# Kernel optimization log

Measured on AMD Instinct MI355X. Metric: run time of the kernel, lower is better.

Reference implementation:

```python
import jax, jax.numpy as jnp
import numpy as np

HEADS = 16
HEAD_DIM = 64
EMBED = HEADS * HEAD_DIM  # 1024
N, L = 4, 4096


def setup_inputs() -> dict:
    key = jax.random.key(0)
    k1, k2, k3, k4, k5, k6, k7, k8 = jax.random.split(key, 8)
    s = 0.02
    return {
        "q": jax.random.normal(k1, (N, L, EMBED), jnp.float32),
        "k": jax.random.normal(k2, (N, L, EMBED), jnp.float32),
        "v": jax.random.normal(k3, (N, L, EMBED), jnp.float32),
        "mask": jnp.ones((N, L, HEADS, HEADS), jnp.int32),
        # torch Linear weights: (out_features, in_features)
        "q_w": jax.random.normal(k4, (HEAD_DIM, HEAD_DIM), jnp.float32) * s,
        "k_w": jax.random.normal(k5, (HEAD_DIM, HEAD_DIM), jnp.float32) * s,
        "v_w": jax.random.normal(k6, (HEAD_DIM, HEAD_DIM), jnp.float32) * s,
        "fc_w": jax.random.normal(k7, (EMBED, EMBED), jnp.float32) * s,
        "fc_b": jax.random.normal(k8, (EMBED,), jnp.float32) * s,
    }


def reference(q, k, v, mask, q_w, k_w, v_w, fc_w, fc_b):
    n, ql = q.shape[0], q.shape[1]
    # reshape to (N, L, H, D) and apply per-head-dim linear projections (x @ W.T)
    q4 = q.reshape(n, ql, HEADS, HEAD_DIM) @ q_w.T
    k4 = k.reshape(n, k.shape[1], HEADS, HEAD_DIM) @ k_w.T
    v4 = v.reshape(n, v.shape[1], HEADS, HEAD_DIM) @ v_w.T
    # Faithful to the original: matmul broadcasts over (N, L), contracting head_dim,
    # so logits are (N, L, H, H) -- attention across heads per token.
    scale = 1.0 / jnp.sqrt(jnp.float32(HEAD_DIM))
    logits = jnp.einsum("nlhd,nlgd->nlhg", q4, k4) * scale
    logits = jnp.where(mask == 0, -jnp.inf, logits)
    weights = jax.nn.softmax(logits, axis=-1)
    out4 = jnp.einsum("nlhg,nlgd->nlhd", weights, v4)  # (N, L, H, D)
    # Faithful scrambled reshape: permute to (N, H, L, D) then flatten to (N, L, H*D)
    out = out4.transpose(0, 2, 1, 3).reshape(n, ql, HEADS * HEAD_DIM)
    return out @ fc_w.T + fc_b
```

## Files before the change

kernel.cpp:

```cpp
#include <hip/hip_runtime.h>
#include <hip/hip_bf16.h>
#include <stdint.h>

#define TOKENS 16384
#define LSEQ 4096
#define WPAD 72

typedef short bf16x8 __attribute__((ext_vector_type(8)));
typedef float f32x4 __attribute__((ext_vector_type(4)));

typedef __attribute__((address_space(1))) void as1_t;
typedef __attribute__((address_space(3))) void as3_t;

__device__ __forceinline__ unsigned short f2bf(float x) {
  __hip_bfloat16 t = __float2bfloat16(x);
  return *reinterpret_cast<unsigned short*>(&t);
}

__device__ __forceinline__ bf16x8 pack8(float4 a, float4 b) {
  bf16x8 t;
  t[0] = (short)f2bf(a.x); t[1] = (short)f2bf(a.y);
  t[2] = (short)f2bf(a.z); t[3] = (short)f2bf(a.w);
  t[4] = (short)f2bf(b.x); t[5] = (short)f2bf(b.y);
  t[6] = (short)f2bf(b.z); t[7] = (short)f2bf(b.w);
  return t;
}

__device__ __forceinline__ void async16(const void* g, void* lds) {
  __builtin_amdgcn_global_load_lds((as1_t*)const_cast<void*>(g),
                                   (as3_t*)lds, 16, 0, 0);
}

__global__ __launch_bounds__(256) void cvt_bf16(const float* __restrict__ s,
                                                unsigned short* __restrict__ d,
                                                int n4) {
  int i = blockIdx.x * 256 + threadIdx.x;
  if (i < n4) {
    float4 f = ((const float4*)s)[i];
    union { unsigned short us[4]; uint2 u2; } pk;
    pk.us[0] = f2bf(f.x); pk.us[1] = f2bf(f.y);
    pk.us[2] = f2bf(f.z); pk.us[3] = f2bf(f.w);
    ((uint2*)d)[i] = pk.u2;
  }
}

__global__ __launch_bounds__(1024) void prep_weights(
    const float* __restrict__ qw, const float* __restrict__ kw,
    const float* __restrict__ vw, unsigned short* __restrict__ Mout,
    unsigned short* __restrict__ vwout) {
  __shared__ float ql[4096], kl[4096];
  const int t = threadIdx.x;
  ((float4*)ql)[t] = ((const float4*)qw)[t];
  ((float4*)kl)[t] = ((const float4*)kw)[t];
  {
    float4 f = ((const float4*)vw)[t];
    union { unsigned short us[4]; uint2 u2; } pk;
    pk.us[0] = f2bf(f.x); pk.us[1] = f2bf(f.y);
    pk.us[2] = f2bf(f.z); pk.us[3] = f2bf(f.w);
    ((uint2*)vwout)[t] = pk.u2;
  }
  __syncthreads();
  const int f = t >> 4;
  const int e0 = (t & 15) * 4;
  float acc0 = 0.f, acc1 = 0.f, acc2 = 0.f, acc3 = 0.f;
#pragma unroll 8
  for (int d = 0; d < 64; ++d) {
    const float qv = ql[d * 64 + f];
    const float4 kv = *(const float4*)&kl[d * 64 + e0];
    acc0 += qv * kv.x; acc1 += qv * kv.y; acc2 += qv * kv.z; acc3 += qv * kv.w;
  }
  union { unsigned short us[4]; uint2 u2; } pk;
  pk.us[0] = f2bf(acc0); pk.us[1] = f2bf(acc1);
  pk.us[2] = f2bf(acc2); pk.us[3] = f2bf(acc3);
  *(uint2*)&Mout[f * 64 + e0] = pk.u2;
}

#define STG_BYTES 13312

__global__ __launch_bounds__(128) void attn7(
    const float* __restrict__ q, const float* __restrict__ k,
    const float* __restrict__ v, const int* __restrict__ mask,
    const unsigned short* __restrict__ Mg, const unsigned short* __restrict__ vwg,
    unsigned short* __restrict__ X) {
  __shared__ unsigned short Ml[64 * WPAD];
  __shared__ unsigned short Vw[64 * WPAD];
  __shared__ char stg_[2][2][STG_BYTES];
  __shared__ char scr_[2][2048];

  const int tid = threadIdx.x;
  const int l = tid & 63, w = tid >> 6;
  const int lr = l & 15, lg = l >> 4;
  char* scr = scr_[w];

  {
    const int row = tid >> 1, c0 = (tid & 1) * 32;
#pragma unroll
    for (int j = 0; j < 4; ++j) {
      *(uint4*)&Ml[row * WPAD + c0 + j * 8] = *(const uint4*)(Mg + row * 64 + c0 + j * 8);
      *(uint4*)&Vw[row * WPAD + c0 + j * 8] = *(const uint4*)(vwg + row * 64 + c0 + j * 8);
    }
  }
  __syncthreads();

  auto issue = [&](int tok, char* dst) {
    const size_t tb = (size_t)tok * 1024;
#pragma unroll
    for (int i = 0; i < 4; ++i) {
      const int r = i * 4 + (l >> 4);
      const int se = r * 64 + (((l & 15) ^ (r & 7)) << 2);
      async16(q + tb + se, dst + i * 1024);
      async16(k + tb + se, dst + 4096 + i * 1024);
      async16(v + tb + se, dst + 8192 + i * 1024);
    }
    async16(mask + (size_t)tok * 256 + l * 4, dst + 12288);
  };

  const int tok0 = (blockIdx.x * 2 + w) * 8;
  issue(tok0, stg_[w][0]);

  const int r7 = lr & 7;
  const int fr0 = lr * 128 + ((lg * 16) ^ (r7 << 4));
  const int fr1 = lr * 128 + ((64 + lg * 16) ^ (r7 << 4));

#pragma unroll
  for (int t = 0; t < 8; ++t) {
    const int tok = tok0 + t;
    char* cur = stg_[w][t & 1];

    if (t < 7) {
      issue(tok + 1, stg_[w][(t + 1) & 1]);
      asm volatile("s_waitcnt vmcnt(13)" ::: "memory");
    } else {
      asm volatile("s_waitcnt vmcnt(2)" ::: "memory");
    }
    __builtin_amdgcn_sched_barrier(0);

    const int4 mk4 = *(const int4*)(cur + 12288 + lr * 64 + lg * 16);
    auto ldfrag = [&](const char* base, int kc) -> bf16x8 {
      const int c0 = kc * 8 + 2 * lg;
      const float4 f0 = *(const float4*)(base + lr * 256 + (((c0) ^ r7) << 4));
      const float4 f1 = *(const float4*)(base + lr * 256 + (((c0 + 1) ^ r7) << 4));
      return pack8(f0, f1);
    };
    const bf16x8 aq0 = ldfrag(cur, 0),        aq1 = ldfrag(cur, 1);
    const bf16x8 ak0 = ldfrag(cur + 4096, 0), ak1 = ldfrag(cur + 4096, 1);
    const bf16x8 av0 = ldfrag(cur + 8192, 0), av1 = ldfrag(cur + 8192, 1);

    f32x4 accu[4], accv[4];
#pragma unroll
    for (int n = 0; n < 4; ++n) {
      const int wrow = (n * 16 + lr) * WPAD;
      f32x4 z = {};
      const bf16x8 bm0 = *(const bf16x8*)&Ml[wrow + lg * 8];
      const bf16x8 bm1 = *(const bf16x8*)&Ml[wrow + 32 + lg * 8];
      accu[n] = __builtin_amdgcn_mfma_f32_16x16x32_bf16(ak0, bm0, z, 0, 0, 0);
      accu[n] = __builtin_amdgcn_mfma_f32_16x16x32_bf16(ak1, bm1, accu[n], 0, 0, 0);
      const bf16x8 bw0 = *(const bf16x8*)&Vw[wrow + lg * 8];
      const bf16x8 bw1 = *(const bf16x8*)&Vw[wrow + 32 + lg * 8];
      accv[n] = __builtin_amdgcn_mfma_f32_16x16x32_bf16(av0, bw0, z, 0, 0, 0);
      accv[n] = __builtin_amdgcn_mfma_f32_16x16x32_bf16(av1, bw1, accv[n], 0, 0, 0);
    }

#pragma unroll
    for (int n = 0; n < 4; ++n)
#pragma unroll
      for (int r = 0; r < 4; ++r) {
        const int row = lg * 4 + r;
        *(unsigned short*)(scr + row * 128 + ((32 * n + 2 * lr) ^ ((row & 7) << 4))) =
            f2bf(accu[n][r]);
      }
    const bf16x8 ua0 = *(const bf16x8*)(scr + fr0);
    const bf16x8 ua1 = *(const bf16x8*)(scr + fr1);
    f32x4 z4 = {};
    f32x4 st = __builtin_amdgcn_mfma_f32_16x16x32_bf16(ua0, aq0, z4, 0, 0, 0);
    st = __builtin_amdgcn_mfma_f32_16x16x32_bf16(ua1, aq1, st, 0, 0, 0);

    float e[4];
    float sm = 0.f;
    const int mks[4] = {mk4.x, mk4.y, mk4.z, mk4.w};
#pragma unroll
    for (int r = 0; r < 4; ++r) {
      e[r] = (mks[r] != 0) ? __expf(st[r] * 0.125f) : 0.f;
      sm += e[r];
    }
    sm += __shfl_xor(sm, 16);
    sm += __shfl_xor(sm, 32);
    const float inv = 1.0f / sm;
#pragma unroll
    for (int r = 0; r < 4; ++r) e[r] *= inv;

    bf16x8 apv;
#pragma unroll
    for (int j = 0; j < 8; ++j) {
      const int srcg = (lg * 2 + (j >> 2)) & 3;
      const float pv = __shfl(e[j & 3], lr + srcg * 16, 64);
      apv[j] = (short)((lg < 2) ? f2bf(pv) : (unsigned short)0);
    }

    const int s0 = lr + ((lg & 1) * 2) * 16;
    const int s1 = s0 + 16;
    f32x4 o[4];
#pragma unroll
    for (int n = 0; n < 4; ++n) {
      bf16x8 bv;
#pragma unroll
      for (int j = 0; j < 8; ++j) {
        const float xv = __shfl(accv[n][j & 3], (j < 4) ? s0 : s1, 64);
        bv[j] = (short)f2bf(xv);
      }
      f32x4 z = {};
      o[n] = __builtin_amdgcn_mfma_f32_16x16x32_bf16(apv, bv, z, 0, 0, 0);
    }

#pragma unroll
    for (int n = 0; n < 4; ++n)
#pragma unroll
      for (int r = 0; r < 4; ++r) {
        const int row = lg * 4 + r;
        *(unsigned short*)(scr + row * 128 + ((32 * n + 2 * lr) ^ ((row & 7) << 4))) =
            f2bf(o[n][r]);
      }
    const int nb = tok >> 12, lpos = tok & (LSEQ - 1);
#pragma unroll
    for (int it = 0; it < 2; ++it) {
      const int idx = it * 64 + l;
      const int h = idx >> 3, c = idx & 7;
      const uint4 val = *(const uint4*)(scr + h * 128 + ((c * 16) ^ ((h & 7) << 4)));
      *(uint4*)&X[((size_t)(nb * 16 + h) * LSEQ + lpos) * 64 + c * 8] = val;
    }
  }
}

__global__ __launch_bounds__(256) void gemm_fc(const unsigned short* __restrict__ A,
                                               const unsigned short* __restrict__ B,
                                               const float* __restrict__ bias,
                                               float* __restrict__ C) {
  __shared__ unsigned short sA[128 * 32];
  __shared__ unsigned short sB[128 * 32];
  const int tid = threadIdx.x;
  const int l = tid & 63, w = tid >> 6;
  const int wr = w >> 1, wc = w & 1;

  const int bid = blockIdx.x;
  const int wg = (bid & 7) * 128 + (bid >> 3);
  const int tm = (wg >> 3) * 128;
  const int tn = (wg & 7) * 128;

  f32x4 acc[4][4] = {};

  const int r0 = w * 16 + (l >> 2);
  const int c8 = (l & 3) * 8;

  for (int kt = 0; kt < 32; ++kt) {
    const int k0 = kt * 32;
#pragma unroll
    for (int s = 0; s < 2; ++s) {
      async16(A + (size_t)(tm + s * 64 + r0) * 1024 + k0 + c8,
              (char*)sA + s * 4096 + w * 1024);
      async16(B + (size_t)(tn + s * 64 + r0) * 1024 + k0 + c8,
              (char*)sB + s * 4096 + w * 1024);
    }
    __syncthreads();

    bf16x8 af[4], bfr[4];
#pragma unroll
    for (int fi = 0; fi < 4; ++fi)
      af[fi] = *(const bf16x8*)((const char*)sA +
                                (wr * 64 + fi * 16 + (l & 15)) * 64 + (l >> 4) * 16);
#pragma unroll
    for (int fj = 0; fj < 4; ++fj)
      bfr[fj] = *(const bf16x8*)((const char*)sB +
                                 (wc * 64 + fj * 16 + (l & 15)) * 64 + (l >> 4) * 16);
#pragma unroll
    for (int fi = 0; fi < 4; ++fi)
#pragma unroll
      for (int fj = 0; fj < 4; ++fj)
        acc[fi][fj] = __builtin_amdgcn_mfma_f32_16x16x32_bf16(af[fi], bfr[fj],
                                                              acc[fi][fj], 0, 0, 0);
    __syncthreads();
  }

#pragma unroll
  for (int fj = 0; fj < 4; ++fj) {
    const int col = tn + wc * 64 + fj * 16 + (l & 15);
    const float bv = bias[col];
#pragma unroll
    for (int fi = 0; fi < 4; ++fi) {
#pragma unroll
      for (int r = 0; r < 4; ++r) {
        const int row = tm + wr * 64 + fi * 16 + (l >> 4) * 4 + r;
        C[(size_t)row * 1024 + col] = acc[fi][fj][r] + bv;
      }
    }
  }
}

extern "C" void kernel_launch(void* const* d_in, const int* in_sizes, int n_in,
                              void* d_out, int out_size, void* d_ws, size_t ws_size,
                              hipStream_t stream) {
  (void)in_sizes; (void)n_in; (void)out_size; (void)ws_size;
  const float* q   = (const float*)d_in[0];
  const float* k   = (const float*)d_in[1];
  const float* v   = (const float*)d_in[2];
  const int*  mask = (const int*)d_in[3];
  const float* qw  = (const float*)d_in[4];
  const float* kw  = (const float*)d_in[5];
  const float* vw  = (const float*)d_in[6];
  const float* fcw = (const float*)d_in[7];
  const float* fcb = (const float*)d_in[8];
  float* out = (float*)d_out;

  unsigned short* X   = (unsigned short*)d_ws;
  unsigned short* Wb  = X + (size_t)16 * 1024 * 1024;
  unsigned short* Mw  = Wb + (size_t)1024 * 1024;
  unsigned short* vwb = Mw + 4096;

  cvt_bf16<<<dim3(1024), dim3(256), 0, stream>>>(fcw, Wb, 262144);
  prep_weights<<<dim3(1), dim3(1024), 0, stream>>>(qw, kw, vw, Mw, vwb);
  attn7<<<dim3(1024), dim3(128), 0, stream>>>(q, k, v, mask, Mw, vwb, X);
  gemm_fc<<<dim3(1024), dim3(256), 0, stream>>>(X, Wb, fcb, out);
}
```

Before: 120.6 us.

## Replace LDS async staging with register-prefetched global loads in attention kernel

Result: faster. 116.1 us (-3.7%).

```diff
diff --git a/kernel.cpp b/kernel.cpp
--- a/kernel.cpp
+++ b/kernel.cpp
@@ -5,6 +5,7 @@
 #define TOKENS 16384
 #define LSEQ 4096
 #define WPAD 72
+#define NT 4
 
 typedef short bf16x8 __attribute__((ext_vector_type(8)));
 typedef float f32x4 __attribute__((ext_vector_type(4)));
@@ -30,6 +31,19 @@
   __builtin_amdgcn_global_load_lds((as1_t*)const_cast<void*>(g),
                                    (as3_t*)lds, 16, 0, 0);
 }
+
+__device__ __forceinline__ float4 aload(const float* p) {
+  float4 r;
+  asm volatile("global_load_dwordx4 %0, %1, off" : "=v"(r) : "v"(p));
+  return r;
+}
+__device__ __forceinline__ int4 aloadi(const int* p) {
+  int4 r;
+  asm volatile("global_load_dwordx4 %0, %1, off" : "=v"(r) : "v"(p));
+  return r;
+}
+#define WAITCNT(n) asm volatile("s_waitcnt vmcnt(" #n ")" ::: "memory")
+#define SBAR() __builtin_amdgcn_sched_barrier(0)
 
 __global__ __launch_bounds__(256) void cvt_bf16(const float* __restrict__ s,
                                                 unsigned short* __restrict__ d,
@@ -75,88 +89,88 @@
   *(uint2*)&Mout[f * 64 + e0] = pk.u2;
 }
 
-#define STG_BYTES 13312
-
-__global__ __launch_bounds__(128) void attn7(
+__global__ __launch_bounds__(256) void attn8(
     const float* __restrict__ q, const float* __restrict__ k,
     const float* __restrict__ v, const int* __restrict__ mask,
     const unsigned short* __restrict__ Mg, const unsigned short* __restrict__ vwg,
     unsigned short* __restrict__ X) {
-  __shared__ unsigned short Ml[64 * WPAD];
-  __shared__ unsigned short Vw[64 * WPAD];
-  __shared__ char stg_[2][2][STG_BYTES];
-  __shared__ char scr_[2][2048];
+  __shared__ char Mlb[8192];
+  __shared__ char Vwb[8192];
+  __shared__ char scr_[4][2048];
 
   const int tid = threadIdx.x;
   const int l = tid & 63, w = tid >> 6;
   const int lr = l & 15, lg = l >> 4;
   char* scr = scr_[w];
 
-  {
-    const int row = tid >> 1, c0 = (tid & 1) * 32;
-#pragma unroll
-    for (int j = 0; j < 4; ++j) {
-      *(uint4*)&Ml[row * WPAD + c0 + j * 8] = *(const uint4*)(Mg + row * 64 + c0 + j * 8);
-      *(uint4*)&Vw[row * WPAD + c0 + j * 8] = *(const uint4*)(vwg + row * 64 + c0 + j * 8);
-    }
+#pragma unroll
+  for (int i = 0; i < 2; ++i) {
+    const int idx = tid + i * 256;
+    const int row = idx >> 3, c = idx & 7;
+    const int dst = row * 128 + ((c * 16) ^ ((row & 7) << 4));
+    *(uint4*)(Mlb + dst) = *(const uint4*)(Mg + row * 64 + c * 8);
+    *(uint4*)(Vwb + dst) = *(const uint4*)(vwg + row * 64 + c * 8);
   }
   __syncthreads();
 
-  auto issue = [&](int tok, char* dst) {
-    const size_t tb = (size_t)tok * 1024;
-#pragma unroll
-    for (int i = 0; i < 4; ++i) {
-      const int r = i * 4 + (l >> 4);
-      const int se = r * 64 + (((l & 15) ^ (r & 7)) << 2);
-      async16(q + tb + se, dst + i * 1024);
-      async16(k + tb + se, dst + 4096 + i * 1024);
-      async16(v + tb + se, dst + 8192 + i * 1024);
-    }
-    async16(mask + (size_t)tok * 256 + l * 4, dst + 12288);
-  };
-
-  const int tok0 = (blockIdx.x * 2 + w) * 8;
-  issue(tok0, stg_[w][0]);
-
   const int r7 = lr & 7;
+  const int wc0 = (lg * 16) ^ (r7 << 4);
+  const int wc1 = (64 + lg * 16) ^ (r7 << 4);
   const int fr0 = lr * 128 + ((lg * 16) ^ (r7 << 4));
   const int fr1 = lr * 128 + ((64 + lg * 16) ^ (r7 << 4));
-
-#pragma unroll
-  for (int t = 0; t < 8; ++t) {
+  const int off = lr * 64 + lg * 8;
+
+  const int tok0 = (blockIdx.x * 4 + w) * NT;
+
+  float4 L[12];
+  int4 Lm;
+  {
+    const size_t tb = (size_t)tok0 * 1024;
+    L[0] = aload(q + tb + off);      L[1] = aload(q + tb + off + 4);
+    L[2] = aload(q + tb + off + 32); L[3] = aload(q + tb + off + 36);
+    L[4] = aload(k + tb + off);      L[5] = aload(k + tb + off + 4);
+    L[6] = aload(k + tb + off + 32); L[7] = aload(k + tb + off + 36);
+    L[8] = aload(v + tb + off);      L[9] = aload(v + tb + off + 4);
+    L[10] = aload(v + tb + off + 32); L[11] = aload(v + tb + off + 36);
+    Lm = aloadi(mask + (size_t)tok0 * 256 + lr * 16 + lg * 4);
+  }
+
+#pragma unroll
+  for (int t = 0; t < NT; ++t) {
     const int tok = tok0 + t;
-    char* cur = stg_[w][t & 1];
-
-    if (t < 7) {
-      issue(tok + 1, stg_[w][(t + 1) & 1]);
-      asm volatile("s_waitcnt vmcnt(13)" ::: "memory");
-    } else {
-      asm volatile("s_waitcnt vmcnt(2)" ::: "memory");
-    }
-    __builtin_amdgcn_sched_barrier(0);
-
-    const int4 mk4 = *(const int4*)(cur + 12288 + lr * 64 + lg * 16);
-    auto ldfrag = [&](const char* base, int kc) -> bf16x8 {
-      const int c0 = kc * 8 + 2 * lg;
-      const float4 f0 = *(const float4*)(base + lr * 256 + (((c0) ^ r7) << 4));
-      const float4 f1 = *(const float4*)(base + lr * 256 + (((c0 + 1) ^ r7) << 4));
-      return pack8(f0, f1);
-    };
-    const bf16x8 aq0 = ldfrag(cur, 0),        aq1 = ldfrag(cur, 1);
-    const bf16x8 ak0 = ldfrag(cur + 4096, 0), ak1 = ldfrag(cur + 4096, 1);
-    const bf16x8 av0 = ldfrag(cur + 8192, 0), av1 = ldfrag(cur + 8192, 1);
+
+    if (t == 0) { WAITCNT(0); } else { WAITCNT(2); }
+    SBAR();
+
+    const bf16x8 aq0 = pack8(L[0], L[1]),  aq1 = pack8(L[2], L[3]);
+    const bf16x8 ak0 = pack8(L[4], L[5]),  ak1 = pack8(L[6], L[7]);
+    const bf16x8 av0 = pack8(L[8], L[9]),  av1 = pack8(L[10], L[11]);
+    const int4 mk4 = Lm;
+    SBAR();
+
+    if (t < NT - 1) {
+      const size_t tb = (size_t)(tok + 1) * 1024;
+      L[0] = aload(q + tb + off);      L[1] = aload(q + tb + off + 4);
+      L[2] = aload(q + tb + off + 32); L[3] = aload(q + tb + off + 36);
+      L[4] = aload(k + tb + off);      L[5] = aload(k + tb + off + 4);
+      L[6] = aload(k + tb + off + 32); L[7] = aload(k + tb + off + 36);
+      L[8] = aload(v + tb + off);      L[9] = aload(v + tb + off + 4);
+      L[10] = aload(v + tb + off + 32); L[11] = aload(v + tb + off + 36);
+      Lm = aloadi(mask + (size_t)(tok + 1) * 256 + lr * 16 + lg * 4);
+    }
+    SBAR();
 
     f32x4 accu[4], accv[4];
 #pragma unroll
     for (int n = 0; n < 4; ++n) {
-      const int wrow = (n * 16 + lr) * WPAD;
+      const int wrow = (n * 16 + lr) * 128;
       f32x4 z = {};
-      const bf16x8 bm0 = *(const bf16x8*)&Ml[wrow + lg * 8];
-      const bf16x8 bm1 = *(const bf16x8*)&Ml[wrow + 32 + lg * 8];
+      const bf16x8 bm0 = *(const bf16x8*)(Mlb + wrow + wc0);
+      const bf16x8 bm1 = *(const bf16x8*)(Mlb + wrow + wc1);
       accu[n] = __builtin_amdgcn_mfma_f32_16x16x32_bf16(ak0, bm0, z, 0, 0, 0);
       accu[n] = __builtin_amdgcn_mfma_f32_16x16x32_bf16(ak1, bm1, accu[n], 0, 0, 0);
-      const bf16x8 bw0 = *(const bf16x8*)&Vw[wrow + lg * 8];
-      const bf16x8 bw1 = *(const bf16x8*)&Vw[wrow + 32 + lg * 8];
+      const bf16x8 bw0 = *(const bf16x8*)(Vwb + wrow + wc0);
+      const bf16x8 bw1 = *(const bf16x8*)(Vwb + wrow + wc1);
       accv[n] = __builtin_amdgcn_mfma_f32_16x16x32_bf16(av0, bw0, z, 0, 0, 0);
       accv[n] = __builtin_amdgcn_mfma_f32_16x16x32_bf16(av1, bw1, accv[n], 0, 0, 0);
     }
@@ -317,6 +331,6 @@
 
   cvt_bf16<<<dim3(1024), dim3(256), 0, stream>>>(fcw, Wb, 262144);
   prep_weights<<<dim3(1), dim3(1024), 0, stream>>>(qw, kw, vw, Mw, vwb);
-  attn7<<<dim3(1024), dim3(128), 0, stream>>>(q, k, v, mask, Mw, vwb, X);
+  attn8<<<dim3(1024), dim3(256), 0, stream>>>(q, k, v, mask, Mw, vwb, X);
   gemm_fc<<<dim3(1024), dim3(256), 0, stream>>>(X, Wb, fcb, out);
 }
```

## Use producer-consumer warp specialization in attention kernel and merge weight prep kernels

Applied to the files above, without the earlier changes.

After: 115.1 us. 4.5% less time.

```diff
diff --git a/kernel.cpp b/kernel.cpp
--- a/kernel.cpp
+++ b/kernel.cpp
@@ -4,7 +4,8 @@
 
 #define TOKENS 16384
 #define LSEQ 4096
-#define WPAD 72
+#define ROUNDS 16
+#define SLOT 13312
 
 typedef short bf16x8 __attribute__((ext_vector_type(8)));
 typedef float f32x4 __attribute__((ext_vector_type(4)));
@@ -31,83 +32,90 @@
                                    (as3_t*)lds, 16, 0, 0);
 }
 
-__global__ __launch_bounds__(256) void cvt_bf16(const float* __restrict__ s,
-                                                unsigned short* __restrict__ d,
-                                                int n4) {
-  int i = blockIdx.x * 256 + threadIdx.x;
-  if (i < n4) {
-    float4 f = ((const float4*)s)[i];
+__global__ __launch_bounds__(256) void cvt_prep(
+    const float* __restrict__ fcw, unsigned short* __restrict__ Wb,
+    const float* __restrict__ qw, const float* __restrict__ kw,
+    const float* __restrict__ vw, unsigned short* __restrict__ Mout,
+    unsigned short* __restrict__ vwout) {
+  const int b = blockIdx.x, t = threadIdx.x;
+  if (b < 1024) {
+    const int i = b * 256 + t;
+    float4 f = ((const float4*)fcw)[i];
     union { unsigned short us[4]; uint2 u2; } pk;
     pk.us[0] = f2bf(f.x); pk.us[1] = f2bf(f.y);
     pk.us[2] = f2bf(f.z); pk.us[3] = f2bf(f.w);
-    ((uint2*)d)[i] = pk.u2;
-  }
-}
-
-__global__ __launch_bounds__(1024) void prep_weights(
-    const float* __restrict__ qw, const float* __restrict__ kw,
-    const float* __restrict__ vw, unsigned short* __restrict__ Mout,
-    unsigned short* __restrict__ vwout) {
+    ((uint2*)Wb)[i] = pk.u2;
+    return;
+  }
   __shared__ float ql[4096], kl[4096];
-  const int t = threadIdx.x;
-  ((float4*)ql)[t] = ((const float4*)qw)[t];
-  ((float4*)kl)[t] = ((const float4*)kw)[t];
-  {
-    float4 f = ((const float4*)vw)[t];
+#pragma unroll
+  for (int j = 0; j < 4; ++j) {
+    const int i = t + j * 256;
+    ((float4*)ql)[i] = ((const float4*)qw)[i];
+    ((float4*)kl)[i] = ((const float4*)kw)[i];
+    float4 f = ((const float4*)vw)[i];
     union { unsigned short us[4]; uint2 u2; } pk;
     pk.us[0] = f2bf(f.x); pk.us[1] = f2bf(f.y);
     pk.us[2] = f2bf(f.z); pk.us[3] = f2bf(f.w);
-    ((uint2*)vwout)[t] = pk.u2;
+    ((uint2*)vwout)[i] = pk.u2;
   }
   __syncthreads();
-  const int f = t >> 4;
-  const int e0 = (t & 15) * 4;
-  float acc0 = 0.f, acc1 = 0.f, acc2 = 0.f, acc3 = 0.f;
+  const int f = t >> 2;
+  const int e0 = (t & 3) * 16;
+  float4 a0 = {}, a1 = {}, a2 = {}, a3 = {};
 #pragma unroll 8
   for (int d = 0; d < 64; ++d) {
     const float qv = ql[d * 64 + f];
-    const float4 kv = *(const float4*)&kl[d * 64 + e0];
-    acc0 += qv * kv.x; acc1 += qv * kv.y; acc2 += qv * kv.z; acc3 += qv * kv.w;
-  }
-  union { unsigned short us[4]; uint2 u2; } pk;
-  pk.us[0] = f2bf(acc0); pk.us[1] = f2bf(acc1);
-  pk.us[2] = f2bf(acc2); pk.us[3] = f2bf(acc3);
-  *(uint2*)&Mout[f * 64 + e0] = pk.u2;
-}
-
-#define STG_BYTES 13312
-
-__global__ __launch_bounds__(128) void attn7(
+    const float* kr = &kl[d * 64 + e0];
+    const float4 k0 = *(const float4*)(kr);
+    const float4 k1 = *(const float4*)(kr + 4);
+    const float4 k2 = *(const float4*)(kr + 8);
+    const float4 k3 = *(const float4*)(kr + 12);
+    a0.x += qv * k0.x; a0.y += qv * k0.y; a0.z += qv * k0.z; a0.w += qv * k0.w;
+    a1.x += qv * k1.x; a1.y += qv * k1.y; a1.z += qv * k1.z; a1.w += qv * k1.w;
+    a2.x += qv * k2.x; a2.y += qv * k2.y; a2.z += qv * k2.z; a2.w += qv * k2.w;
+    a3.x += qv * k3.x; a3.y += qv * k3.y; a3.z += qv * k3.z; a3.w += qv * k3.w;
+  }
+  union { unsigned short us[8]; uint4 u4; } p0, p1;
+  p0.us[0] = f2bf(a0.x); p0.us[1] = f2bf(a0.y); p0.us[2] = f2bf(a0.z); p0.us[3] = f2bf(a0.w);
+  p0.us[4] = f2bf(a1.x); p0.us[5] = f2bf(a1.y); p0.us[6] = f2bf(a1.z); p0.us[7] = f2bf(a1.w);
+  p1.us[0] = f2bf(a2.x); p1.us[1] = f2bf(a2.y); p1.us[2] = f2bf(a2.z); p1.us[3] = f2bf(a2.w);
+  p1.us[4] = f2bf(a3.x); p1.us[5] = f2bf(a3.y); p1.us[6] = f2bf(a3.z); p1.us[7] = f2bf(a3.w);
+  *(uint4*)&Mout[f * 64 + e0] = p0.u4;
+  *(uint4*)&Mout[f * 64 + e0 + 8] = p1.u4;
+}
+
+__global__ __launch_bounds__(384, 1) void attn_pc(
     const float* __restrict__ q, const float* __restrict__ k,
     const float* __restrict__ v, const int* __restrict__ mask,
     const unsigned short* __restrict__ Mg, const unsigned short* __restrict__ vwg,
     unsigned short* __restrict__ X) {
-  __shared__ unsigned short Ml[64 * WPAD];
-  __shared__ unsigned short Vw[64 * WPAD];
-  __shared__ char stg_[2][2][STG_BYTES];
-  __shared__ char scr_[2][2048];
+  __shared__ char Mlb[8192];
+  __shared__ char Vwb[8192];
+  __shared__ char buf[2][4][SLOT];
+  __shared__ char scr_[4][2048];
 
   const int tid = threadIdx.x;
   const int l = tid & 63, w = tid >> 6;
   const int lr = l & 15, lg = l >> 4;
-  char* scr = scr_[w];
-
-  {
-    const int row = tid >> 1, c0 = (tid & 1) * 32;
-#pragma unroll
-    for (int j = 0; j < 4; ++j) {
-      *(uint4*)&Ml[row * WPAD + c0 + j * 8] = *(const uint4*)(Mg + row * 64 + c0 + j * 8);
-      *(uint4*)&Vw[row * WPAD + c0 + j * 8] = *(const uint4*)(vwg + row * 64 + c0 + j * 8);
-    }
+  const int r7 = lr & 7;
+
+  for (int idx = tid; idx < 512; idx += 384) {
+    const int row = idx >> 3, c = idx & 7;
+    const int dst = row * 128 + ((c * 16) ^ ((row & 7) << 4));
+    *(uint4*)(Mlb + dst) = *(const uint4*)(Mg + row * 64 + c * 8);
+    *(uint4*)(Vwb + dst) = *(const uint4*)(vwg + row * 64 + c * 8);
   }
   __syncthreads();
 
-  auto issue = [&](int tok, char* dst) {
+  const int tok0 = blockIdx.x * 64;
+
+  auto issue_slot = [&](int tok, char* dst) {
     const size_t tb = (size_t)tok * 1024;
 #pragma unroll
     for (int i = 0; i < 4; ++i) {
-      const int r = i * 4 + (l >> 4);
-      const int se = r * 64 + (((l & 15) ^ (r & 7)) << 2);
+      const int row = i * 4 + (l >> 4);
+      const int se = row * 64 + (((l & 15) ^ (row & 7)) << 2);
       async16(q + tb + se, dst + i * 1024);
       async16(k + tb + se, dst + 4096 + i * 1024);
       async16(v + tb + se, dst + 8192 + i * 1024);
@@ -115,119 +123,125 @@
     async16(mask + (size_t)tok * 256 + l * 4, dst + 12288);
   };
 
-  const int tok0 = (blockIdx.x * 2 + w) * 8;
-  issue(tok0, stg_[w][0]);
-
-  const int r7 = lr & 7;
-  const int fr0 = lr * 128 + ((lg * 16) ^ (r7 << 4));
-  const int fr1 = lr * 128 + ((64 + lg * 16) ^ (r7 << 4));
-
-#pragma unroll
-  for (int t = 0; t < 8; ++t) {
-    const int tok = tok0 + t;
-    char* cur = stg_[w][t & 1];
-
-    if (t < 7) {
-      issue(tok + 1, stg_[w][(t + 1) & 1]);
-      asm volatile("s_waitcnt vmcnt(13)" ::: "memory");
+  if (w < 2) {
+#pragma unroll
+    for (int si = w * 2; si < w * 2 + 2; ++si)
+      issue_slot(tok0 + si, buf[0][si]);
+    asm volatile("s_waitcnt vmcnt(0)" ::: "memory");
+  }
+  __syncthreads();
+
+  for (int r = 0; r < ROUNDS; ++r) {
+    if (w < 2) {
+      if (r < ROUNDS - 1) {
+#pragma unroll
+        for (int si = w * 2; si < w * 2 + 2; ++si)
+          issue_slot(tok0 + (r + 1) * 4 + si, buf[(r + 1) & 1][si]);
+        asm volatile("s_waitcnt vmcnt(0)" ::: "memory");
+      }
     } else {
-      asm volatile("s_waitcnt vmcnt(2)" ::: "memory");
+      const int cw = w - 2;
+      const int tok = tok0 + r * 4 + cw;
+      char* slot = buf[r & 1][cw];
+      char* scr = scr_[cw];
+
+      const int4 mk4 = *(const int4*)(slot + 12288 + lr * 64 + lg * 16);
+      auto ldfrag = [&](const char* base, int kc) -> bf16x8 {
+        const int c0 = kc * 8 + 2 * lg;
+        const float4 f0 = *(const float4*)(base + lr * 256 + ((c0 ^ r7) << 4));
+        const float4 f1 = *(const float4*)(base + lr * 256 + (((c0 + 1) ^ r7) << 4));
+        return pack8(f0, f1);
+      };
+      const bf16x8 aq0 = ldfrag(slot, 0),        aq1 = ldfrag(slot, 1);
+      const bf16x8 ak0 = ldfrag(slot + 4096, 0), ak1 = ldfrag(slot + 4096, 1);
+      const bf16x8 av0 = ldfrag(slot + 8192, 0), av1 = ldfrag(slot + 8192, 1);
+
+      const int wc0 = (lg * 16) ^ (r7 << 4);
+      const int wc1 = (64 + lg * 16) ^ (r7 << 4);
+      f32x4 accu[4], accv[4];
+#pragma unroll
+      for (int n = 0; n < 4; ++n) {
+        const int wrow = (n * 16 + lr) * 128;
+        f32x4 z = {};
+        const bf16x8 bm0 = *(const bf16x8*)(Mlb + wrow + wc0);
+        const bf16x8 bm1 = *(const bf16x8*)(Mlb + wrow + wc1);
+        accu[n] = __builtin_amdgcn_mfma_f32_16x16x32_bf16(ak0, bm0, z, 0, 0, 0);
+        accu[n] = __builtin_amdgcn_mfma_f32_16x16x32_bf16(ak1, bm1, accu[n], 0, 0, 0);
+        const bf16x8 bw0 = *(const bf16x8*)(Vwb + wrow + wc0);
+        const bf16x8 bw1 = *(const bf16x8*)(Vwb + wrow + wc1);
+        accv[n] = __builtin_amdgcn_mfma_f32_16x16x32_bf16(av0, bw0, z, 0, 0, 0);
+        accv[n] = __builtin_amdgcn_mfma_f32_16x16x32_bf16(av1, bw1, accv[n], 0, 0, 0);
+      }
+
+#pragma unroll
+      for (int n = 0; n < 4; ++n)
+#pragma unroll
+        for (int rr = 0; rr < 4; ++rr) {
+          const int row = lg * 4 + rr;
+          *(unsigned short*)(scr + row * 128 + ((32 * n + 2 * lr) ^ ((row & 7) << 4))) =
+              f2bf(accu[n][rr]);
+        }
+      const bf16x8 ua0 = *(const bf16x8*)(scr + lr * 128 + ((lg * 16) ^ (r7 << 4)));
+      const bf16x8 ua1 = *(const bf16x8*)(scr + lr * 128 + ((64 + lg * 16) ^ (r7 << 4)));
+      f32x4 z4 = {};
+      f32x4 st = __builtin_amdgcn_mfma_f32_16x16x32_bf16(ua0, aq0, z4, 0, 0, 0);
+      st = __builtin_amdgcn_mfma_f32_16x16x32_bf16(ua1, aq1, st, 0, 0, 0);
+
+      float e[4];
+      float sm = 0.f;
+      const int mks[4] = {mk4.x, mk4.y, mk4.z, mk4.w};
+#pragma unroll
+      for (int rr = 0; rr < 4; ++rr) {
+        e[rr] = (mks[rr] != 0) ? __expf(st[rr] * 0.125f) : 0.f;
+        sm += e[rr];
+      }
+      sm += __shfl_xor(sm, 16);
+      sm += __shfl_xor(sm, 32);
+      const float inv = 1.0f / sm;
+#pragma unroll
+      for (int rr = 0; rr < 4; ++rr) e[rr] *= inv;
+
+      bf16x8 apv;
+#pragma unroll
+      for (int j = 0; j < 8; ++j) {
+        const int srcg = (lg * 2 + (j >> 2)) & 3;
+        const float pv = __shfl(e[j & 3], lr + srcg * 16, 64);
+        apv[j] = (short)((lg < 2) ? f2bf(pv) : (unsigned short)0);
+      }
+
+      const int s0 = lr + ((lg & 1) * 2) * 16;
+      const int s1 = s0 + 16;
+      f32x4 o[4];
+#pragma unroll
+      for (int n = 0; n < 4; ++n) {
+        bf16x8 bv;
+#pragma unroll
+        for (int j = 0; j < 8; ++j) {
+          const float xv = __shfl(accv[n][j & 3], (j < 4) ? s0 : s1, 64);
+          bv[j] = (short)f2bf(xv);
+        }
+        f32x4 z = {};
+        o[n] = __builtin_amdgcn_mfma_f32_16x16x32_bf16(apv, bv, z, 0, 0, 0);
+      }
+
+#pragma unroll
+      for (int n = 0; n < 4; ++n)
+#pragma unroll
+        for (int rr = 0; rr < 4; ++rr) {
+          const int row = lg * 4 + rr;
+          *(unsigned short*)(scr + row * 128 + ((32 * n + 2 * lr) ^ ((row & 7) << 4))) =
+              f2bf(o[n][rr]);
+        }
+      const int nb = tok >> 12, lpos = tok & (LSEQ - 1);
+#pragma unroll
+      for (int it = 0; it < 2; ++it) {
+        const int idx = it * 64 + l;
+        const int h = idx >> 3, c = idx & 7;
+        const uint4 val = *(const uint4*)(scr + h * 128 + ((c * 16) ^ ((h & 7) << 4)));
+        *(uint4*)&X[((size_t)(nb * 16 + h) * LSEQ + lpos) * 64 + c * 8] = val;
+      }
     }
-    __builtin_amdgcn_sched_barrier(0);
-
-    const int4 mk4 = *(const int4*)(cur + 12288 + lr * 64 + lg * 16);
-    auto ldfrag = [&](const char* base, int kc) -> bf16x8 {
-      const int c0 = kc * 8 + 2 * lg;
-      const float4 f0 = *(const float4*)(base + lr * 256 + (((c0) ^ r7) << 4));
-      const float4 f1 = *(const float4*)(base + lr * 256 + (((c0 + 1) ^ r7) << 4));
-      return pack8(f0, f1);
-    };
-    const bf16x8 aq0 = ldfrag(cur, 0),        aq1 = ldfrag(cur, 1);
-    const bf16x8 ak0 = ldfrag(cur + 4096, 0), ak1 = ldfrag(cur + 4096, 1);
-    const bf16x8 av0 = ldfrag(cur + 8192, 0), av1 = ldfrag(cur + 8192, 1);
-
-    f32x4 accu[4], accv[4];
-#pragma unroll
-    for (int n = 0; n < 4; ++n) {
-      const int wrow = (n * 16 + lr) * WPAD;
-      f32x4 z = {};
-      const bf16x8 bm0 = *(const bf16x8*)&Ml[wrow + lg * 8];
-      const bf16x8 bm1 = *(const bf16x8*)&Ml[wrow + 32 + lg * 8];
-      accu[n] = __builtin_amdgcn_mfma_f32_16x16x32_bf16(ak0, bm0, z, 0, 0, 0);
-      accu[n] = __builtin_amdgcn_mfma_f32_16x16x32_bf16(ak1, bm1, accu[n], 0, 0, 0);
-      const bf16x8 bw0 = *(const bf16x8*)&Vw[wrow + lg * 8];
-      const bf16x8 bw1 = *(const bf16x8*)&Vw[wrow + 32 + lg * 8];
-      accv[n] = __builtin_amdgcn_mfma_f32_16x16x32_bf16(av0, bw0, z, 0, 0, 0);
-      accv[n] = __builtin_amdgcn_mfma_f32_16x16x32_bf16(av1, bw1, accv[n], 0, 0, 0);
-    }
-
-#pragma unroll
-    for (int n = 0; n < 4; ++n)
-#pragma unroll
-      for (int r = 0; r < 4; ++r) {
-        const int row = lg * 4 + r;
-        *(unsigned short*)(scr + row * 128 + ((32 * n + 2 * lr) ^ ((row & 7) << 4))) =
-            f2bf(accu[n][r]);
-      }
-    const bf16x8 ua0 = *(const bf16x8*)(scr + fr0);
-    const bf16x8 ua1 = *(const bf16x8*)(scr + fr1);
-    f32x4 z4 = {};
-    f32x4 st = __builtin_amdgcn_mfma_f32_16x16x32_bf16(ua0, aq0, z4, 0, 0, 0);
-    st = __builtin_amdgcn_mfma_f32_16x16x32_bf16(ua1, aq1, st, 0, 0, 0);
-
-    float e[4];
-    float sm = 0.f;
-    const int mks[4] = {mk4.x, mk4.y, mk4.z, mk4.w};
-#pragma unroll
-    for (int r = 0; r < 4; ++r) {
-      e[r] = (mks[r] != 0) ? __expf(st[r] * 0.125f) : 0.f;
-      sm += e[r];
-    }
-    sm += __shfl_xor(sm, 16);
-    sm += __shfl_xor(sm, 32);
-    const float inv = 1.0f / sm;
-#pragma unroll
-    for (int r = 0; r < 4; ++r) e[r] *= inv;
-
-    bf16x8 apv;
-#pragma unroll
-    for (int j = 0; j < 8; ++j) {
-      const int srcg = (lg * 2 + (j >> 2)) & 3;
-      const float pv = __shfl(e[j & 3], lr + srcg * 16, 64);
-      apv[j] = (short)((lg < 2) ? f2bf(pv) : (unsigned short)0);
-    }
-
-    const int s0 = lr + ((lg & 1) * 2) * 16;
-    const int s1 = s0 + 16;
-    f32x4 o[4];
-#pragma unroll
-    for (int n = 0; n < 4; ++n) {
-      bf16x8 bv;
-#pragma unroll
-      for (int j = 0; j < 8; ++j) {
-        const float xv = __shfl(accv[n][j & 3], (j < 4) ? s0 : s1, 64);
-        bv[j] = (short)f2bf(xv);
-      }
-      f32x4 z = {};
-      o[n] = __builtin_amdgcn_mfma_f32_16x16x32_bf16(apv, bv, z, 0, 0, 0);
-    }
-
-#pragma unroll
-    for (int n = 0; n < 4; ++n)
-#pragma unroll
-      for (int r = 0; r < 4; ++r) {
-        const int row = lg * 4 + r;
-        *(unsigned short*)(scr + row * 128 + ((32 * n + 2 * lr) ^ ((row & 7) << 4))) =
-            f2bf(o[n][r]);
-      }
-    const int nb = tok >> 12, lpos = tok & (LSEQ - 1);
-#pragma unroll
-    for (int it = 0; it < 2; ++it) {
-      const int idx = it * 64 + l;
-      const int h = idx >> 3, c = idx & 7;
-      const uint4 val = *(const uint4*)(scr + h * 128 + ((c * 16) ^ ((h & 7) << 4)));
-      *(uint4*)&X[((size_t)(nb * 16 + h) * LSEQ + lpos) * 64 + c * 8] = val;
-    }
+    __syncthreads();
   }
 }
 
@@ -315,8 +329,7 @@
   unsigned short* Mw  = Wb + (size_t)1024 * 1024;
   unsigned short* vwb = Mw + 4096;
 
-  cvt_bf16<<<dim3(1024), dim3(256), 0, stream>>>(fcw, Wb, 262144);
-  prep_weights<<<dim3(1), dim3(1024), 0, stream>>>(qw, kw, vw, Mw, vwb);
-  attn7<<<dim3(1024), dim3(128), 0, stream>>>(q, k, v, mask, Mw, vwb, X);
+  cvt_prep<<<dim3(1025), dim3(256), 0, stream>>>(fcw, Wb, qw, kw, vw, Mw, vwb);
+  attn_pc<<<dim3(256), dim3(384), 0, stream>>>(q, k, v, mask, Mw, vwb, X);
   gemm_fc<<<dim3(1024), dim3(256), 0, stream>>>(X, Wb, fcb, out);
 }
```
